# Optimization experiments

Hardware: AMD Instinct MI355X
Metric: run time of the kernel (lower is better)

The kernel has to match this reference:

```python
import jax, jax.numpy as jnp
import numpy as np

B, D_IN, M, D_MEM = 65536, 64, 2048, 64


def setup_inputs() -> dict:
    key = jax.random.key(0)
    k = jax.random.split(key, 5)
    glorot = lambda kk, shape: jax.random.uniform(
        kk, shape, jnp.float32,
        -jnp.sqrt(6.0 / (shape[0] + shape[1])), jnp.sqrt(6.0 / (shape[0] + shape[1])))
    return {
        "inputs": jax.random.normal(k[0], (B, D_IN), jnp.float32),
        "W_att": glorot(k[1], (D_IN, M)),
        "b_att": jnp.zeros((M,), jnp.float32),
        "W_write": glorot(k[2], (D_IN, D_MEM)),
        "b_write": jnp.zeros((D_MEM,), jnp.float32),
        "memory": glorot(k[3], (M, D_MEM)),
        "update_gate": jnp.full((M,), 0.5, jnp.float32),
    }


def reference(inputs, W_att, b_att, W_write, b_write, memory, update_gate):
    # Read attention: Dense(memory_size, softmax) -> [B, M]
    read_attention = jax.nn.softmax(inputs @ W_att + b_att, axis=-1)
    # Read: [B, M] @ [M, Dm] -> [B, Dm]
    read_vector = read_attention @ memory
    # Write candidate: Dense(memory_dim, tanh) -> [B, Dm]
    candidate_write = jnp.tanh(inputs @ W_write + b_write)
    aggregated_write = jnp.mean(candidate_write, axis=0)[None, :]  # [1, Dm]
    write_attention = jnp.mean(read_attention, axis=0)             # [M]
    update_weights = (write_attention * update_gate)[:, None]      # [M, 1]
    # Gated in-place memory update (returned as new state)
    new_memory = memory * (1.0 - update_weights) + update_weights * aggregated_write
    return read_vector, new_memory
```

## Files before the change

kernel.cpp:

```cpp
#include <hip/hip_runtime.h>
#include <hip/hip_bf16.h>

typedef unsigned int   u32;
typedef unsigned short u16;

typedef __bf16 bf16x8 __attribute__((ext_vector_type(8)));
typedef float  f32x4  __attribute__((ext_vector_type(4)));
typedef u32    u32x4  __attribute__((ext_vector_type(4)));
typedef u32    u32x2  __attribute__((ext_vector_type(2)));

union Frag { u32x4 u; bf16x8 b; };

#define MFMA16 __builtin_amdgcn_mfma_f32_16x16x32_bf16

#define B_ROWS 65536
#define D_IN   64
#define M_SZ   2048
#define D_MEM  64

#define WT_OFF      0
#define MEMT_OFF    262144
#define WWT_OFF     524288
#define CSF_OFF     532480
#define AGF_OFF     540672
#define CSP_OFF     540928
#define AGP_OFF     8929536
#define WS_REQUIRED 9191680

#define L2E 1.4426950408889634f

__device__ __forceinline__ float bf2f(u16 h) { return __uint_as_float(((u32)h) << 16); }
__device__ __forceinline__ u16 f2bf(float f) {
    u32 u = __float_as_uint(f);
    return (u16)((u + 0x7FFFu + ((u >> 16) & 1u)) >> 16);
}
#if defined(__has_builtin) && __has_builtin(__builtin_amdgcn_exp2f)
__device__ __forceinline__ float exp2fast(float x) { return __builtin_amdgcn_exp2f(x); }
#else
__device__ __forceinline__ float exp2fast(float x) { return __expf(x * 0.6931471805599453f); }
#endif
__device__ __forceinline__ float tanh_fast(float x) {
    const float e = exp2fast(x * (2.0f * L2E));
    return 1.0f - 2.0f * __builtin_amdgcn_rcpf(e + 1.0f);
}
__device__ __forceinline__ bool detect_bf16(const void* ug) {
    return ((const u32*)ug)[0] == 0x3F003F00u;
}
__device__ __forceinline__ float load_elem(const void* p, size_t i, bool isbf) {
    return isbf ? bf2f(((const u16*)p)[i]) : ((const float*)p)[i];
}

__device__ __forceinline__ u32 cvtpk_bf16(float lo, float hi) {
    u32 r;
    asm("v_cvt_pk_bf16_f32 %0, %1, %2" : "=v"(r) : "v"(lo), "v"(hi));
    return r;
}
#if defined(__has_builtin) && __has_builtin(__builtin_amdgcn_permlane32_swap) && \
    __has_builtin(__builtin_amdgcn_permlane16_swap)
__device__ __forceinline__ void pl32swap(u32& a, u32& b) {
    u32x2 r = __builtin_amdgcn_permlane32_swap(a, b, false, false);
    a = r[0]; b = r[1];
}
__device__ __forceinline__ void pl16swap(u32& a, u32& b) {
    u32x2 r = __builtin_amdgcn_permlane16_swap(a, b, false, false);
    a = r[0]; b = r[1];
}
#else
__device__ __forceinline__ void pl32swap(u32& a, u32& b) {
    asm("v_permlane32_swap_b32 %0, %1" : "+v"(a), "+v"(b));
}
__device__ __forceinline__ void pl16swap(u32& a, u32& b) {
    asm("v_permlane16_swap_b32 %0, %1" : "+v"(a), "+v"(b));
}
#endif
template<int CTRL>
__device__ __forceinline__ float xadd(float v) {
    int x = __builtin_amdgcn_update_dpp(0, __float_as_int(v), CTRL, 0xF, 0xF, true);
    return v + __int_as_float(x);
}

__global__ void __launch_bounds__(256)
prep_kernel(const void* Watt, const void* mem_in, const void* Wwr, const void* ug,
            u16* Wt, u16* memT, u16* Wwt, float* CSF)
{
    const bool isbf = detect_bf16(ug);
    const int b = blockIdx.x;
    const int t = threadIdx.x;
    if (b == 65) {
        for (int i = t; i < 2112; i += 256) CSF[i] = 0.f;
        return;
    }
    __shared__ u16 tile[64][65];
    const void* src; u16* dst; int R, C, rb, cb;
    if (b < 32)      { src = Watt;   dst = Wt;   R = 64;   C = 2048; rb = 0;           cb = b * 64; }
    else if (b < 64) { src = mem_in; dst = memT; R = 2048; C = 64;   rb = (b-32) * 64; cb = 0;      }
    else             { src = Wwr;    dst = Wwt;  R = 64;   C = 64;   rb = 0;           cb = 0;      }

#pragma unroll
    for (int j = 0; j < 16; ++j) {
        int e = j * 256 + t;
        int r = e >> 6, c = e & 63;
        float v = load_elem(src, (size_t)(rb + r) * C + cb + c, isbf);
        tile[r][c] = f2bf(v);
    }
    __syncthreads();
#pragma unroll
    for (int j = 0; j < 16; ++j) {
        int e = j * 256 + t;
        int c2 = e >> 6, r2 = e & 63;
        dst[(size_t)(cb + c2) * R + rb + r2] = tile[r2][c2];
    }
}

__global__ void __launch_bounds__(256, 2)
main_kernel(const void* x_in, const void* batt_in, const void* bwrite_in,
            const u16* __restrict__ Wt, const u16* __restrict__ memT,
            const u16* __restrict__ Wwt, const void* ug,
            float* CSF, float* AGF, u16* cs_part, u16* ag_part,
            int use_part, void* out)
{
    const bool isbf = detect_bf16(ug);
    const int tid = threadIdx.x;
    const int lane = tid & 63, wave = tid >> 6;
    const int quad = lane >> 4, l4 = lane & 15;
    const int rowbase = blockIdx.x * 128;
    const int wrow = blockIdx.x * 4 + wave;

    __shared__ __align__(16) u16 WtC[256][72];
    __shared__ __align__(16) u16 MeC[64][264];
    __shared__ __align__(16) float battL[2048];

    {
        const int i0 = tid * 8;
#pragma unroll
        for (int j = 0; j < 8; ++j)
            battL[i0 + j] = load_elem(batt_in, i0 + j, isbf) * L2E;
    }

    auto stageWtC = [&](int ch) {
        const char* src = (const char*)(Wt + (size_t)ch * 16384);
#pragma unroll
        for (int j = 0; j < 8; ++j) {
            const int o = j * 4096 + tid * 16;
            const int m = o >> 7, k8 = (o & 127) >> 1;
            u32x4 v = *(const u32x4*)(src + o);
            *(u32x4*)&WtC[m][k8] = v;
        }
    };
    auto stageMeC = [&](int ch) {
#pragma unroll
        for (int j = 0; j < 8; ++j) {
            const int d = j * 8 + (tid >> 5);
            const int mo = (tid & 31) * 8;
            const u16* g = memT + (size_t)d * 2048 + ch * 256 + mo;
            u32x4 v = *(const u32x4*)g;
            *(u32x4*)&MeC[d][mo] = v;
        }
    };

    Frag a[2][2];
#pragma unroll
    for (int rg = 0; rg < 2; ++rg) {
        const int arow = rowbase + wave * 32 + rg * 16 + l4;
        if (isbf) {
            const u16* xp = (const u16*)x_in + (size_t)arow * 64 + quad * 8;
            a[rg][0].u = *(const u32x4*)xp;
            a[rg][1].u = *(const u32x4*)(xp + 32);
        } else {
            const float* xp = (const float*)x_in + (size_t)arow * 64 + quad * 8;
#pragma unroll
            for (int j = 0; j < 8; ++j) {
                ((u16*)&a[rg][0])[j] = f2bf(xp[j]);
                ((u16*)&a[rg][1])[j] = f2bf(xp[32 + j]);
            }
        }
    }
    const f32x4 zf = {0.f, 0.f, 0.f, 0.f};

    stageWtC(0);

    float agout = 0.f;
    {
        f32x4 accW[4][2];
#pragma unroll
        for (int t = 0; t < 4; ++t) {
            const u16* bp = Wwt + (size_t)(t * 16 + l4) * 64 + quad * 8;
            Frag b0, b1; b0.u = *(const u32x4*)bp; b1.u = *(const u32x4*)(bp + 32);
#pragma unroll
            for (int rg = 0; rg < 2; ++rg) {
                accW[t][rg] = MFMA16(a[rg][0].b, b0.b, zf, 0, 0, 0);
                accW[t][rg] = MFMA16(a[rg][1].b, b1.b, accW[t][rg], 0, 0, 0);
            }
        }
#pragma unroll
        for (int t = 0; t < 4; ++t) {
            const float bw = load_elem(bwrite_in, t * 16 + l4, isbf);
            float s = 0.f;
#pragma unroll
            for (int rg = 0; rg < 2; ++rg)
#pragma unroll
                for (int i = 0; i < 4; ++i) s += tanh_fast(accW[t][rg][i] + bw);
            s += __shfl_xor(s, 16, 64);
            s += __shfl_xor(s, 32, 64);
            if (quad == t) agout = s;
        }
    }
    if (use_part) ag_part[wrow * 64 + lane] = f2bf(agout);
    else          atomicAdd(&AGF[lane], agout);

    __syncthreads();

    float lsum[2] = {0.f, 0.f};
    for (int ch = 0; ch < 8; ++ch) {
        for (int cc = 0; cc < 4; ++cc) {
            const int mb = cc * 64;
            const int mbase = ch * 256 + mb;
            Frag wb0[4], wb1[4]; f32x4 blv[4];
#pragma unroll
            for (int t = 0; t < 4; ++t) {
                wb0[t].u = *(const u32x4*)&WtC[mb + t * 16 + l4][quad * 8];
                wb1[t].u = *(const u32x4*)&WtC[mb + t * 16 + l4][32 + quad * 8];
                blv[t] = *(const f32x4*)&battL[mbase + t * 16 + quad * 4];
            }
#pragma unroll
            for (int t = 0; t < 4; ++t)
#pragma unroll
                for (int rg = 0; rg < 2; ++rg) {
                    f32x4 acc = MFMA16(wb0[t].b, a[rg][0].b, zf, 0, 0, 0);
                    acc = MFMA16(wb1[t].b, a[rg][1].b, acc, 0, 0, 0);
#pragma unroll
                    for (int i = 0; i < 4; ++i)
                        lsum[rg] += exp2fast(fmaf(acc[i], L2E, blv[t][i]));
                }
        }
        __syncthreads();
        if (ch < 7) { stageWtC(ch + 1); __syncthreads(); }
    }
    float invl[2];
#pragma unroll
    for (int rg = 0; rg < 2; ++rg) {
        float v = lsum[rg];
        v += __shfl_xor(v, 16, 64);
        v += __shfl_xor(v, 32, 64);
        invl[rg] = 1.f / v;
    }

    f32x4 oaccT[2][4] = {{zf,zf,zf,zf},{zf,zf,zf,zf}};
    stageMeC(7);
    __syncthreads();
    const bool sb0 = (l4 & 1), sb1 = (l4 & 2), sb2 = (l4 & 4), sb3 = (l4 & 8);
    for (int ch = 7; ch >= 0; --ch) {
        for (int cc = 0; cc < 4; ++cc) {
            const int mb = cc * 64;
            const int mbase = ch * 256 + mb;
            Frag wb0[4], wb1[4], mb0[4], mb1[4]; f32x4 blv[4];
#pragma unroll
            for (int t = 0; t < 4; ++t) {
                wb0[t].u = *(const u32x4*)&WtC[mb + t * 16 + l4][quad * 8];
                wb1[t].u = *(const u32x4*)&WtC[mb + t * 16 + l4][32 + quad * 8];
                mb0[t].u = *(const u32x4*)&MeC[t * 16 + l4][mb + quad * 8];
                mb1[t].u = *(const u32x4*)&MeC[t * 16 + l4][mb + 32 + quad * 8];
                blv[t] = *(const f32x4*)&battL[mbase + t * 16 + quad * 4];
            }
            u32 P0[2][4], P1[2][4];
            float c16[16];
#pragma unroll
            for (int j = 0; j < 16; ++j) c16[j] = 0.f;
#pragma unroll
            for (int t = 0; t < 4; ++t)
#pragma unroll
                for (int rg = 0; rg < 2; ++rg) {
                    f32x4 acc = MFMA16(wb0[t].b, a[rg][0].b, zf, 0, 0, 0);
                    acc = MFMA16(wb1[t].b, a[rg][1].b, acc, 0, 0, 0);
                    const float il = invl[rg];
                    const float e0 = exp2fast(fmaf(acc[0], L2E, blv[t][0]));
                    const float e1 = exp2fast(fmaf(acc[1], L2E, blv[t][1]));
                    const float e2 = exp2fast(fmaf(acc[2], L2E, blv[t][2]));
                    const float e3 = exp2fast(fmaf(acc[3], L2E, blv[t][3]));
                    c16[t * 4 + 0] = fmaf(e0, il, c16[t * 4 + 0]);
                    c16[t * 4 + 1] = fmaf(e1, il, c16[t * 4 + 1]);
                    c16[t * 4 + 2] = fmaf(e2, il, c16[t * 4 + 2]);
                    c16[t * 4 + 3] = fmaf(e3, il, c16[t * 4 + 3]);
                    P0[rg][t] = cvtpk_bf16(e0, e1);
                    P1[rg][t] = cvtpk_bf16(e2, e3);
                }
#pragma unroll
            for (int rg = 0; rg < 2; ++rg)
#pragma unroll
                for (int cc2 = 0; cc2 < 2; ++cc2) {
                    u32 b0 = P0[rg][2 * cc2], b2 = P0[rg][2 * cc2 + 1];
                    u32 b1 = P1[rg][2 * cc2], b3 = P1[rg][2 * cc2 + 1];
                    pl32swap(b0, b2); pl16swap(b0, b2);
                    pl32swap(b1, b3); pl16swap(b1, b3);
                    Frag bf; bf.u = (u32x4){b0, b1, b2, b3};
#pragma unroll
                    for (int dt = 0; dt < 4; ++dt) {
                        if (cc2 == 0)
                            oaccT[rg][dt] = MFMA16(mb0[dt].b, bf.b, oaccT[rg][dt], 0, 0, 0);
                        else
                            oaccT[rg][dt] = MFMA16(mb1[dt].b, bf.b, oaccT[rg][dt], 0, 0, 0);
                    }
                }
            float u8[8];
#pragma unroll
            for (int k = 0; k < 8; ++k) {
                const float t0 = xadd<0xB1>(c16[2 * k]);
                const float t1 = xadd<0xB1>(c16[2 * k + 1]);
                u8[k] = sb0 ? t1 : t0;
            }
            float v4[4];
#pragma unroll
            for (int k = 0; k < 4; ++k) {
                const float t0 = xadd<0x4E>(u8[2 * k]);
                const float t1 = xadd<0x4E>(u8[2 * k + 1]);
                v4[k] = sb1 ? t1 : t0;
            }
            float w2[2];
#pragma unroll
            for (int k = 0; k < 2; ++k) {
                const float t0 = xadd<0x128>(v4[2 * k]);
                const float t1 = xadd<0x128>(v4[2 * k + 1]);
                w2[k] = sb3 ? t1 : t0;
            }
            const float f0 = w2[0] + __shfl_xor(w2[0], 4, 64);
            const float f1 = w2[1] + __shfl_xor(w2[1], 4, 64);
            const float csv = sb2 ? f1 : f0;
            const int tsel = ((l4 >> 3) & 1) | (((l4 >> 2) & 1) << 1);
            const int mout = mbase + tsel * 16 + quad * 4 + (l4 & 3);
            if (use_part) cs_part[(size_t)wrow * 2048 + mout] = f2bf(csv);
            else          atomicAdd(&CSF[mout], csv);
        }
        __syncthreads();
        if (ch > 0) { stageWtC(ch - 1); stageMeC(ch - 1); __syncthreads(); }
    }

#pragma unroll
    for (int rg = 0; rg < 2; ++rg)
#pragma unroll
        for (int dt = 0; dt < 4; ++dt) {
            const int gr = rowbase + wave * 32 + rg * 16 + l4;
            const int d0 = dt * 16 + quad * 4;
            const f32x4 o = oaccT[rg][dt] * invl[rg];
            if (isbf) {
                u32x2 w;
                w.x = cvtpk_bf16(o[0], o[1]);
                w.y = cvtpk_bf16(o[2], o[3]);
                *(u32x2*)&((u16*)out)[(size_t)gr * 64 + d0] = w;
            } else {
                *(f32x4*)&((float*)out)[(size_t)gr * 64 + d0] = o;
            }
        }
}

__global__ void __launch_bounds__(256)
reduce_kernel(const u16* __restrict__ cs_part, const u16* __restrict__ ag_part,
              float* CSF, float* AGF)
{
    const int b = blockIdx.x, t = threadIdx.x;
    if (b < 64) {
        const int m = (b & 7) * 256 + t;
        const int w0 = (b >> 3) * 256;
        float s = 0.f;
        for (int k = 0; k < 256; ++k) s += bf2f(cs_part[(size_t)(w0 + k) * 2048 + m]);
        atomicAdd(&CSF[m], s);
    } else if (t < 64) {
        const int w0 = (b - 64) * 512;
        float s = 0.f;
        for (int k = 0; k < 512; ++k) s += bf2f(ag_part[(w0 + k) * 64 + t]);
        atomicAdd(&AGF[t], s);
    }
}

__global__ void __launch_bounds__(256)
finalize_kernel(const void* mem_in, const void* ug,
                const float* __restrict__ CSF, const float* __restrict__ AGF,
                void* out)
{
    const bool isbf = detect_bf16(ug);
    const int idx = blockIdx.x * 256 + threadIdx.x;
    const int m = idx >> 6, d = idx & 63;
    const float wa  = CSF[m] * (1.f / 65536.f);
    const float agg = AGF[d] * (1.f / 65536.f);
    const float uw  = wa * load_elem(ug, m, isbf);
    const float mv  = load_elem(mem_in, idx, isbf);
    const float nm  = mv * (1.f - uw) + uw * agg;
    if (isbf) ((u16*)out)[(size_t)4194304 + idx] = f2bf(nm);
    else      ((float*)out)[(size_t)4194304 + idx] = nm;
}

extern "C" void kernel_launch(void* const* d_in, const int* in_sizes, int n_in,
                              void* d_out, int out_size, void* d_ws, size_t ws_size,
                              hipStream_t stream)
{
    (void)in_sizes; (void)n_in; (void)out_size;
    const void* x    = d_in[0];
    const void* Watt = d_in[1];
    const void* batt = d_in[2];
    const void* Wwr  = d_in[3];
    const void* bwr  = d_in[4];
    const void* mem  = d_in[5];
    const void* ug   = d_in[6];

    char* ws = (char*)d_ws;
    u16*   Wt      = (u16*)(ws + WT_OFF);
    u16*   memT    = (u16*)(ws + MEMT_OFF);
    u16*   Wwt     = (u16*)(ws + WWT_OFF);
    float* CSF     = (float*)(ws + CSF_OFF);
    float* AGF     = (float*)(ws + AGF_OFF);
    u16*   cs_part = (u16*)(ws + CSP_OFF);
    u16*   ag_part = (u16*)(ws + AGP_OFF);
    const int use_part = (ws_size >= (size_t)WS_REQUIRED) ? 1 : 0;

    prep_kernel<<<66, 256, 0, stream>>>(Watt, mem, Wwr, ug, Wt, memT, Wwt, CSF);
    main_kernel<<<512, 256, 0, stream>>>(x, batt, bwr, Wt, memT, Wwt, ug,
                                         CSF, AGF, cs_part, ag_part,
                                         use_part, d_out);
    if (use_part)
        reduce_kernel<<<68, 256, 0, stream>>>(cs_part, ag_part, CSF, AGF);
    finalize_kernel<<<512, 256, 0, stream>>>(mem, ug, CSF, AGF, d_out);
}
```

Baseline: 196.3 us.

## Double-buffer LDS staging with direct global-to-LDS loads, XOR swizzle, fuse tail kernels

Changes the prep kernel to write Wt and memT in an XOR-swizzled layout. The main kernel now stages 128-row chunks into double-buffered LDS with global_load_lds, prefetching the next chunk while computing the current one, which drops the extra barrier per chunk. It raises wave priority around the MFMA block and merges the reduce and finalize kernels into a single tail kernel, removing the atomics and one launch. The tail kernel has each of its 64 blocks redo the full ag_part reduction, and the async LDS copies rely on the next barrier for ordering.

Result: no change. 196.3 us (-0.0%).

```diff
diff --git a/kernel.cpp b/kernel.cpp
--- a/kernel.cpp
+++ b/kernel.cpp
@@ -28,6 +28,18 @@
 #define WS_REQUIRED 9191680
 
 #define L2E 1.4426950408889634f
+
+#define AS1 __attribute__((address_space(1)))
+#define AS3 __attribute__((address_space(3)))
+
+#if defined(__has_builtin)
+#if __has_builtin(__builtin_amdgcn_global_load_lds)
+#define HAS_GLD 1
+#endif
+#endif
+#ifndef HAS_GLD
+#define HAS_GLD 0
+#endif
 
 __device__ __forceinline__ float bf2f(u16 h) { return __uint_as_float(((u32)h) << 16); }
 __device__ __forceinline__ u16 f2bf(float f) {
@@ -91,10 +103,10 @@
         return;
     }
     __shared__ u16 tile[64][65];
-    const void* src; u16* dst; int R, C, rb, cb;
-    if (b < 32)      { src = Watt;   dst = Wt;   R = 64;   C = 2048; rb = 0;           cb = b * 64; }
-    else if (b < 64) { src = mem_in; dst = memT; R = 2048; C = 64;   rb = (b-32) * 64; cb = 0;      }
-    else             { src = Wwr;    dst = Wwt;  R = 64;   C = 64;   rb = 0;           cb = 0;      }
+    const void* src; u16* dst; int C, rb, cb, bsel;
+    if (b < 32)      { src = Watt;   dst = Wt;   C = 2048; rb = 0;           cb = b * 64; bsel = 0; }
+    else if (b < 64) { src = mem_in; dst = memT; C = 64;   rb = (b-32) * 64; cb = 0;      bsel = 1; }
+    else             { src = Wwr;    dst = Wwt;  C = 64;   rb = 0;           cb = 0;      bsel = 2; }
 
 #pragma unroll
     for (int j = 0; j < 16; ++j) {
@@ -108,7 +120,18 @@
     for (int j = 0; j < 16; ++j) {
         int e = j * 256 + t;
         int c2 = e >> 6, r2 = e & 63;
-        dst[(size_t)(cb + c2) * R + rb + r2] = tile[r2][c2];
+        size_t di;
+        if (bsel == 0) {
+            const int m = cb + c2;
+            const int k2 = (r2 & 7) | ((((r2 >> 3) ^ m) & 7) << 3);
+            di = (size_t)m * 64 + k2;
+        } else if (bsel == 1) {
+            const int m2 = (r2 & 7) | ((((r2 >> 3) ^ c2) & 7) << 3);
+            di = (size_t)c2 * 2048 + rb + m2;
+        } else {
+            di = (size_t)c2 * 64 + r2;
+        }
+        dst[di] = tile[r2][c2];
     }
 }
 
@@ -126,9 +149,11 @@
     const int rowbase = blockIdx.x * 128;
     const int wrow = blockIdx.x * 4 + wave;
 
-    __shared__ __align__(16) u16 WtC[256][72];
-    __shared__ __align__(16) u16 MeC[64][264];
+    __shared__ __align__(16) u16 WtL[2][128][64];
+    __shared__ __align__(16) u16 MeL[2][64][128];
     __shared__ __align__(16) float battL[2048];
+
+    const int wvu = __builtin_amdgcn_readfirstlane(wave);
 
     {
         const int i0 = tid * 8;
@@ -137,25 +162,30 @@
             battL[i0 + j] = load_elem(batt_in, i0 + j, isbf) * L2E;
     }
 
-    auto stageWtC = [&](int ch) {
-        const char* src = (const char*)(Wt + (size_t)ch * 16384);
-#pragma unroll
-        for (int j = 0; j < 8; ++j) {
-            const int o = j * 4096 + tid * 16;
-            const int m = o >> 7, k8 = (o & 127) >> 1;
-            u32x4 v = *(const u32x4*)(src + o);
-            *(u32x4*)&WtC[m][k8] = v;
-        }
+    auto cp16 = [&](const char* gsrc_lane, char* lds_base_uniform) {
+#if HAS_GLD
+        __builtin_amdgcn_global_load_lds((const AS1 void*)gsrc_lane,
+                                         (AS3 void*)lds_base_uniform, 16, 0, 0);
+#else
+        *(u32x4*)(lds_base_uniform + lane * 16) = *(const u32x4*)gsrc_lane;
+#endif
     };
-    auto stageMeC = [&](int ch) {
-#pragma unroll
-        for (int j = 0; j < 8; ++j) {
-            const int d = j * 8 + (tid >> 5);
-            const int mo = (tid & 31) * 8;
-            const u16* g = memT + (size_t)d * 2048 + ch * 256 + mo;
-            u32x4 v = *(const u32x4*)g;
-            *(u32x4*)&MeC[d][mo] = v;
-        }
+    const char* WtB = (const char*)Wt;
+    const char* MeB = (const char*)memT;
+    auto stageWt = [&](int ch, int b) {
+        char* lb = (char*)&WtL[b][0][0] + wvu * 4096;
+        const char* gb = WtB + (size_t)ch * 16384 + wvu * 4096 + lane * 16;
+#pragma unroll
+        for (int j = 0; j < 4; ++j)
+            cp16(gb + j * 1024, lb + j * 1024);
+    };
+    auto stageMe = [&](int ch, int b) {
+        char* lb = (char*)&MeL[b][0][0] + wvu * 4096;
+        const char* gb = MeB + (size_t)(wvu * 16 + (lane >> 4)) * 4096
+                             + ch * 256 + (lane & 15) * 16;
+#pragma unroll
+        for (int j = 0; j < 4; ++j)
+            cp16(gb + (size_t)j * 16384, lb + j * 1024);
     };
 
     Frag a[2][2];
@@ -177,7 +207,7 @@
     }
     const f32x4 zf = {0.f, 0.f, 0.f, 0.f};
 
-    stageWtC(0);
+    stageWt(0, 0);
 
     float agout = 0.f;
     {
@@ -211,15 +241,18 @@
     __syncthreads();
 
     float lsum[2] = {0.f, 0.f};
-    for (int ch = 0; ch < 8; ++ch) {
-        for (int cc = 0; cc < 4; ++cc) {
-            const int mb = cc * 64;
-            const int mbase = ch * 256 + mb;
+    for (int ch = 0; ch < 16; ++ch) {
+        const int cur = ch & 1;
+        if (ch < 15) stageWt(ch + 1, cur ^ 1);
+        for (int half = 0; half < 2; ++half) {
+            const int mb = half * 64;
+            const int mbase = ch * 128 + mb;
             Frag wb0[4], wb1[4]; f32x4 blv[4];
 #pragma unroll
             for (int t = 0; t < 4; ++t) {
-                wb0[t].u = *(const u32x4*)&WtC[mb + t * 16 + l4][quad * 8];
-                wb1[t].u = *(const u32x4*)&WtC[mb + t * 16 + l4][32 + quad * 8];
+                const int rr = mb + t * 16 + l4, swr = rr & 7;
+                wb0[t].u = *(const u32x4*)&WtL[cur][rr][(quad ^ swr) << 3];
+                wb1[t].u = *(const u32x4*)&WtL[cur][rr][((quad + 4) ^ swr) << 3];
                 blv[t] = *(const f32x4*)&battL[mbase + t * 16 + quad * 4];
             }
 #pragma unroll
@@ -234,7 +267,6 @@
                 }
         }
         __syncthreads();
-        if (ch < 7) { stageWtC(ch + 1); __syncthreads(); }
     }
     float invl[2];
 #pragma unroll
@@ -246,20 +278,25 @@
     }
 
     f32x4 oaccT[2][4] = {{zf,zf,zf,zf},{zf,zf,zf,zf}};
-    stageMeC(7);
+    stageMe(15, 1);
     __syncthreads();
     const bool sb0 = (l4 & 1), sb1 = (l4 & 2), sb2 = (l4 & 4), sb3 = (l4 & 8);
-    for (int ch = 7; ch >= 0; --ch) {
-        for (int cc = 0; cc < 4; ++cc) {
-            const int mb = cc * 64;
-            const int mbase = ch * 256 + mb;
+    for (int ch = 15; ch >= 0; --ch) {
+        const int cur = ch & 1;
+        if (ch > 0) { stageWt(ch - 1, cur ^ 1); stageMe(ch - 1, cur ^ 1); }
+        for (int half = 0; half < 2; ++half) {
+            const int mb = half * 64;
+            const int mbase = ch * 128 + mb;
+            const int mbh8 = mb >> 3;
             Frag wb0[4], wb1[4], mb0[4], mb1[4]; f32x4 blv[4];
 #pragma unroll
             for (int t = 0; t < 4; ++t) {
-                wb0[t].u = *(const u32x4*)&WtC[mb + t * 16 + l4][quad * 8];
-                wb1[t].u = *(const u32x4*)&WtC[mb + t * 16 + l4][32 + quad * 8];
-                mb0[t].u = *(const u32x4*)&MeC[t * 16 + l4][mb + quad * 8];
-                mb1[t].u = *(const u32x4*)&MeC[t * 16 + l4][mb + 32 + quad * 8];
+                const int rr = mb + t * 16 + l4, swr = rr & 7;
+                wb0[t].u = *(const u32x4*)&WtL[cur][rr][(quad ^ swr) << 3];
+                wb1[t].u = *(const u32x4*)&WtL[cur][rr][((quad + 4) ^ swr) << 3];
+                const int dd = t * 16 + l4, swd = dd & 7;
+                mb0[t].u = *(const u32x4*)&MeL[cur][dd][(mbh8 | (quad ^ swd)) << 3];
+                mb1[t].u = *(const u32x4*)&MeL[cur][dd][(mbh8 | ((quad + 4) ^ swd)) << 3];
                 blv[t] = *(const f32x4*)&battL[mbase + t * 16 + quad * 4];
             }
             u32 P0[2][4], P1[2][4];
@@ -284,6 +321,7 @@
                     P0[rg][t] = cvtpk_bf16(e0, e1);
                     P1[rg][t] = cvtpk_bf16(e2, e3);
                 }
+            __builtin_amdgcn_s_setprio(1);
 #pragma unroll
             for (int rg = 0; rg < 2; ++rg)
 #pragma unroll
@@ -301,6 +339,7 @@
                             oaccT[rg][dt] = MFMA16(mb1[dt].b, bf.b, oaccT[rg][dt], 0, 0, 0);
                     }
                 }
+            __builtin_amdgcn_s_setprio(0);
             float u8[8];
 #pragma unroll
             for (int k = 0; k < 8; ++k) {
@@ -331,7 +370,6 @@
             else          atomicAdd(&CSF[mout], csv);
         }
         __syncthreads();
-        if (ch > 0) { stageWtC(ch - 1); stageMeC(ch - 1); __syncthreads(); }
     }
 
 #pragma unroll
@@ -353,21 +391,45 @@
 }
 
 __global__ void __launch_bounds__(256)
-reduce_kernel(const u16* __restrict__ cs_part, const u16* __restrict__ ag_part,
-              float* CSF, float* AGF)
+tail_kernel(const u16* __restrict__ cs_part, const u16* __restrict__ ag_part,
+            const void* mem_in, const void* ug, void* out)
 {
+    const bool isbf = detect_bf16(ug);
     const int b = blockIdx.x, t = threadIdx.x;
-    if (b < 64) {
-        const int m = (b & 7) * 256 + t;
-        const int w0 = (b >> 3) * 256;
+    __shared__ float agL[4][64];
+    __shared__ float csL[32][8];
+    {
+        const int d = t & 63, seg = t >> 6;
         float s = 0.f;
-        for (int k = 0; k < 256; ++k) s += bf2f(cs_part[(size_t)(w0 + k) * 2048 + m]);
-        atomicAdd(&CSF[m], s);
-    } else if (t < 64) {
-        const int w0 = (b - 64) * 512;
+        for (int k = 0; k < 512; ++k)
+            s += bf2f(ag_part[(size_t)(seg * 512 + k) * 64 + d]);
+        agL[seg][d] = s;
+    }
+    {
+        const int m_loc = t >> 3, seg8 = t & 7;
+        const int m = b * 32 + m_loc;
         float s = 0.f;
-        for (int k = 0; k < 512; ++k) s += bf2f(ag_part[(w0 + k) * 64 + t]);
-        atomicAdd(&AGF[t], s);
+        for (int k = 0; k < 256; ++k)
+            s += bf2f(cs_part[(size_t)(seg8 * 256 + k) * 2048 + m]);
+        csL[m_loc][seg8] = s;
+    }
+    __syncthreads();
+    const int m_loc = t >> 3, m = b * 32 + m_loc, d0 = (t & 7) * 8;
+    float cs = 0.f;
+#pragma unroll
+    for (int k = 0; k < 8; ++k) cs += csL[m_loc][k];
+    const float wa = cs * (1.f / 65536.f);
+    const float uw = wa * load_elem(ug, m, isbf);
+#pragma unroll
+    for (int j = 0; j < 8; ++j) {
+        const int d = d0 + j;
+        const float ag = agL[0][d] + agL[1][d] + agL[2][d] + agL[3][d];
+        const float agg = ag * (1.f / 65536.f);
+        const size_t idx = (size_t)m * 64 + d;
+        const float mv = load_elem(mem_in, idx, isbf);
+        const float nm = mv * (1.f - uw) + uw * agg;
+        if (isbf) ((u16*)out)[(size_t)4194304 + idx] = f2bf(nm);
+        else      ((float*)out)[(size_t)4194304 + idx] = nm;
     }
 }
 
@@ -416,6 +478,7 @@
                                          CSF, AGF, cs_part, ag_part,
                                          use_part, d_out);
     if (use_part)
-        reduce_kernel<<<68, 256, 0, stream>>>(cs_part, ag_part, CSF, AGF);
-    finalize_kernel<<<512, 256, 0, stream>>>(mem, ug, CSF, AGF, d_out);
-}
+        tail_kernel<<<64, 256, 0, stream>>>(cs_part, ag_part, mem, ug, d_out);
+    else
+        finalize_kernel<<<512, 256, 0, stream>>>(mem, ug, CSF, AGF, d_out);
+}
```
